# Optimization experiments

Measured on AMD Instinct MI355X. Metric: run time of the kernel, lower is better.

Reference implementation:

```python
import jax, jax.numpy as jnp
import numpy as np

B, T, C = 4, 2048, 1024
N_HEAD = 16
HEAD_DIM = C // N_HEAD
SCALE = 1.0 / np.sqrt(HEAD_DIM).astype(np.float32)


def setup_inputs() -> dict:
    key = jax.random.key(0)
    ks = jax.random.split(key, 5)
    std = 1.0 / np.sqrt(C).astype(np.float32)
    return {
        "x": jax.random.normal(ks[0], (B, T, C), dtype=jnp.float32),
        "Wq": jax.random.normal(ks[1], (C, C), dtype=jnp.float32) * std,
        "Wk": jax.random.normal(ks[2], (C, C), dtype=jnp.float32) * std,
        "Wv": jax.random.normal(ks[3], (C, C), dtype=jnp.float32) * std,
        "Wo": jax.random.normal(ks[4], (C, C), dtype=jnp.float32) * std,
    }


def reference(x, Wq, Wk, Wv, Wo):
    # nn.Linear(x) == x @ W.T; projections then split heads: (B, H, T, D)
    def split_heads(t):
        return t.reshape(B, T, N_HEAD, HEAD_DIM).transpose(0, 2, 1, 3)

    q = split_heads(x @ Wq.T)
    k = split_heads(x @ Wk.T)
    v = split_heads(x @ Wv.T)

    att = jnp.einsum("bhqd,bhkd->bhqk", q, k) * SCALE  # (B, H, T, T)
    causal = jnp.tril(jnp.ones((T, T), dtype=bool))
    att = jnp.where(causal[None, None], att, -jnp.inf)
    att = jax.nn.softmax(att, axis=-1)
    # dropout = 0.0 (eval): identity
    y = jnp.einsum("bhqk,bhkd->bhqd", att, v)  # (B, H, T, D)
    y = y.transpose(0, 2, 1, 3).reshape(B, T, C)
    return y @ Wo.T
```

## Files before the change

kernel.cpp:

```cpp
#include <hip/hip_runtime.h>
#include <stdint.h>

#define B_SZ   4
#define T_SEQ  2048
#define C_DIM  1024
#define N_HEAD 16
#define HEAD_D 64
#define QSCALE 0.18033688011112042f

typedef unsigned short u16;
typedef unsigned int   u32;
typedef __bf16  bfv8  __attribute__((ext_vector_type(8)));
typedef float   f32x4 __attribute__((ext_vector_type(4)));

__device__ __forceinline__ u16 f2bf_hu(float f) {
  union { float f; u32 i; } u; u.f = f;
  return (u16)((u.i + 0x8000u) >> 16);
}
__device__ __forceinline__ u32 pkbf16(float a, float b) {
  union { float f; u32 i; } ua, ub; ua.f = a; ub.f = b;
  return __builtin_amdgcn_perm(ub.i + 0x8000u, ua.i + 0x8000u, 0x07060302u);
}
__device__ __forceinline__ float fexp2(float x) {
#if __has_builtin(__builtin_amdgcn_exp2f)
  return __builtin_amdgcn_exp2f(x);
#else
  return __expf(x * 0.69314718f);
#endif
}

__device__ __forceinline__ void async_cp16(const u16* __restrict__ g, u16* l) {
  __builtin_amdgcn_global_load_lds(
      (const __attribute__((address_space(1))) void*)g,
      (__attribute__((address_space(3))) void*)l, 16, 0, 0);
}

__global__ __launch_bounds__(256) void cvt_all_kernel(
    const float* __restrict__ x,  const float* __restrict__ W0,
    const float* __restrict__ W1, const float* __restrict__ W2,
    const float* __restrict__ W3, u16* __restrict__ dst) {
  int bid = blockIdx.x;
  const float* s; u16* d; int local;
  if (bid < 8192) {
    s = x; d = dst; local = bid;
  } else {
    int w = (bid - 8192) >> 10;
    local  = (bid - 8192) & 1023;
    s = (w == 0) ? W0 : (w == 1) ? W1 : (w == 2) ? W2 : W3;
    d = dst + (size_t)(B_SZ * T_SEQ * C_DIM) + (size_t)w * (C_DIM * C_DIM);
  }
  int i = local * 256 + threadIdx.x;
  float4 v = ((const float4*)s)[i];
  int2 o; o.x = (int)pkbf16(v.x, v.y); o.y = (int)pkbf16(v.z, v.w);
  ((int2*)d)[i] = o;
}

__device__ __forceinline__ void mfma_step(const u16* Sbuf, int wm, int wn,
                                          int frow, int fk, f32x4 acc[4][4]) {
  const u16* As = Sbuf;
  const u16* Bs = Sbuf + 4096;
  bfv8 af[4], bfr[4];
#pragma unroll
  for (int mt = 0; mt < 4; mt++)
    af[mt] = *(const bfv8*)(As + (wm * 64 + mt * 16 + frow) * 32 + fk);
#pragma unroll
  for (int nt = 0; nt < 4; nt++)
    bfr[nt] = *(const bfv8*)(Bs + (wn * 64 + nt * 16 + frow) * 32 + fk);
  __builtin_amdgcn_s_setprio(1);
#pragma unroll
  for (int mt = 0; mt < 4; mt++)
#pragma unroll
    for (int nt = 0; nt < 4; nt++)
      acc[mt][nt] = __builtin_amdgcn_mfma_f32_16x16x32_bf16(
          af[mt], bfr[nt], acc[mt][nt], 0, 0, 0);
  __builtin_amdgcn_s_setprio(0);
}

__device__ __forceinline__ void gemm_core(const u16* __restrict__ A,
                                          const u16* __restrict__ Bw,
                                          int m0, int n0,
                                          f32x4 acc[4][4],
                                          u16* smem) {
  const int tid  = threadIdx.x;
  const int wave = tid >> 6;
  const int lane = tid & 63;
  const int frow = lane & 15;
  const int fk   = (lane >> 4) * 8;
  const int wm   = wave >> 1, wn = wave & 1;

  const int lrow = tid >> 2;
  const int lcol = (tid & 3) * 8;
  const u16* ga0 = A  + (size_t)(m0 + lrow)      * C_DIM + lcol;
  const u16* ga1 = A  + (size_t)(m0 + 64 + lrow) * C_DIM + lcol;
  const u16* gb0 = Bw + (size_t)(n0 + lrow)      * C_DIM + lcol;
  const u16* gb1 = Bw + (size_t)(n0 + 64 + lrow) * C_DIM + lcol;
  u16* b0 = smem;
  u16* b1 = smem + 8192;
  u16* b2 = smem + 16384;
  const int so = tid * 8;

#define STAGE_TO(dst) do {                        \
    async_cp16(ga0, (dst) + so);                  \
    async_cp16(ga1, (dst) + 2048 + so);           \
    async_cp16(gb0, (dst) + 4096 + so);           \
    async_cp16(gb1, (dst) + 6144 + so);           \
    ga0 += 32; ga1 += 32; gb0 += 32; gb1 += 32;   \
  } while (0)
#define WAIT4_BAR do {                                      \
    asm volatile("s_waitcnt vmcnt(4)" ::: "memory");        \
    __builtin_amdgcn_s_barrier();                           \
  } while (0)

  STAGE_TO(b0);
  STAGE_TO(b1);
  WAIT4_BAR;

#pragma unroll 1
  for (int ii = 0; ii < 30; ii += 3) {
    STAGE_TO(b2);
    mfma_step(b0, wm, wn, frow, fk, acc);
    WAIT4_BAR;

    STAGE_TO(b0);
    mfma_step(b1, wm, wn, frow, fk, acc);
    WAIT4_BAR;

    STAGE_TO(b1);
    mfma_step(b2, wm, wn, frow, fk, acc);
    WAIT4_BAR;
  }
  mfma_step(b0, wm, wn, frow, fk, acc);
  asm volatile("s_waitcnt vmcnt(0)" ::: "memory");
  __builtin_amdgcn_s_barrier();
  mfma_step(b1, wm, wn, frow, fk, acc);
#undef STAGE_TO
#undef WAIT4_BAR
}

__global__ __launch_bounds__(256) void gemm_qkv_kernel(
    const u16* __restrict__ X, const u16* __restrict__ Wq,
    const u16* __restrict__ Wk, const u16* __restrict__ Wv,
    u16* __restrict__ Qo, u16* __restrict__ Ko, u16* __restrict__ Vo) {
  __shared__ __align__(16) u16 smem[24576];
  const u16* W = (blockIdx.z == 0) ? Wq : (blockIdx.z == 1) ? Wk : Wv;
  u16* dst     = (blockIdx.z == 0) ? Qo : (blockIdx.z == 1) ? Ko : Vo;
  const int m0 = blockIdx.x * 128, n0 = blockIdx.y * 128;

  f32x4 acc[4][4];
#pragma unroll
  for (int i = 0; i < 4; i++)
#pragma unroll
    for (int j = 0; j < 4; j++) acc[i][j] = {0.f, 0.f, 0.f, 0.f};

  gemm_core(X, W, m0, n0, acc, smem);
  __syncthreads();

  const int lane = threadIdx.x & 63, wave = threadIdx.x >> 6;
  const int wm = wave >> 1, wn = wave & 1;
  const int quad = lane >> 4, col = lane & 15;
  u16* buf = smem + wave * 4096;
  const int bb = (m0 + wm * 64) >> 11;
  const int t0 = (m0 + wm * 64) & (T_SEQ - 1);
  const int h  = (n0 >> 6) + wn;

  if (blockIdx.z == 2) {
#pragma unroll
    for (int mt = 0; mt < 4; mt++)
#pragma unroll
      for (int nt = 0; nt < 4; nt++) {
        int d_l = nt * 16 + col;
        int g   = mt * 4 + quad;
        int gp  = g ^ (d_l & 15);
        int2 o;
        o.x = (int)pkbf16(acc[mt][nt][0], acc[mt][nt][1]);
        o.y = (int)pkbf16(acc[mt][nt][2], acc[mt][nt][3]);
        *(int2*)(buf + d_l * 64 + gp * 4) = o;
      }
#pragma unroll
    for (int tt = 0; tt < 8; tt++) {
      int d_l = tt * 8 + (lane >> 3);
      int seg = lane & 7;
      int g0 = (2 * seg) ^ (d_l & 15), g1 = (2 * seg + 1) ^ (d_l & 15);
      int2 a  = *(const int2*)(buf + d_l * 64 + g0 * 4);
      int2 bv = *(const int2*)(buf + d_l * 64 + g1 * 4);
      int4 o; o.x = a.x; o.y = a.y; o.z = bv.x; o.w = bv.y;
      *(int4*)(Vo + (((size_t)(bb * N_HEAD + h) * HEAD_D + d_l) * T_SEQ
                     + t0 + seg * 8)) = o;
    }
  } else {
    const float sc = (blockIdx.z == 0) ? QSCALE : 1.0f;
#pragma unroll
    for (int mt = 0; mt < 4; mt++)
#pragma unroll
      for (int nt = 0; nt < 4; nt++)
#pragma unroll
        for (int r = 0; r < 4; r++) {
          int m_l = mt * 16 + quad * 4 + r;
          int n_l = nt * 16 + col;
          int gp = (n_l >> 3) ^ (m_l & 7);
          buf[m_l * 64 + gp * 8 + (n_l & 7)] = f2bf_hu(acc[mt][nt][r] * sc);
        }
#pragma unroll
    for (int tt = 0; tt < 8; tt++) {
      int m_l = tt * 8 + (lane >> 3);
      int seg = lane & 7;
      int gp = seg ^ (m_l & 7);
      int4 o = *(const int4*)(buf + m_l * 64 + gp * 8);
      *(int4*)(dst + (((size_t)(bb * N_HEAD + h) * T_SEQ + t0 + m_l) * HEAD_D
                      + seg * 8)) = o;
    }
  }
}

__global__ __launch_bounds__(256) void gemm_out_kernel(
    const u16* __restrict__ Y, const u16* __restrict__ Wo,
    float* __restrict__ Out) {
  __shared__ __align__(16) u16 smem[24576];
  const int m0 = blockIdx.x * 128, n0 = blockIdx.y * 128;

  f32x4 acc[4][4];
#pragma unroll
  for (int i = 0; i < 4; i++)
#pragma unroll
    for (int j = 0; j < 4; j++) acc[i][j] = {0.f, 0.f, 0.f, 0.f};

  gemm_core(Y, Wo, m0, n0, acc, smem);
  __syncthreads();

  const int lane = threadIdx.x & 63, wave = threadIdx.x >> 6;
  const int wm = wave >> 1, wn = wave & 1;
  const int quad = lane >> 4, col = lane & 15;
  float* bufF = (float*)(smem + wave * 4096);

#pragma unroll
  for (int c = 0; c < 2; c++) {
#pragma unroll
    for (int mt = 0; mt < 4; mt++)
#pragma unroll
      for (int nn = 0; nn < 2; nn++)
#pragma unroll
        for (int r = 0; r < 4; r++) {
          int nt = 2 * c + nn;
          int m_l = mt * 16 + quad * 4 + r;
          int n_l = nn * 16 + col;
          int gp = (n_l >> 2) ^ (m_l & 7);
          bufF[m_l * 32 + gp * 4 + (n_l & 3)] = acc[mt][nt][r];
        }
#pragma unroll
    for (int tt = 0; tt < 8; tt++) {
      int m_l = tt * 8 + (lane >> 3);
      int seg = lane & 7;
      int gp = seg ^ (m_l & 7);
      float4 o = *(const float4*)(bufF + m_l * 32 + gp * 4);
      *(float4*)(Out + (size_t)(m0 + wm * 64 + m_l) * C_DIM
                 + n0 + wn * 64 + c * 32 + seg * 4) = o;
    }
  }
}

#define ATT_Q 128

__global__ __launch_bounds__(256, 4) void attn_kernel(
    const u16* __restrict__ Qg, const u16* __restrict__ Kg,
    const u16* __restrict__ Vtg, u16* __restrict__ Yg) {
  __shared__ __align__(16) u16 QPs[128 * 64];
  __shared__ __align__(16) u16 Ks[64 * 64];
  __shared__ __align__(16) u16 Vt[64 * 64];

  const int tid = threadIdx.x;
  const int wave = tid >> 6, lane = tid & 63;
  const int quad = lane >> 4, l15 = lane & 15;
  const int bh = blockIdx.x;
  const int b = bh >> 4, h = bh & 15;
  const int yy = blockIdx.y, gq = yy >> 2, rq = yy & 3;
  const int qt = (gq == 0) ? 15 - rq : (gq == 1) ? rq
               : (gq == 2) ? 11 - rq : 4 + rq;
  const int q0 = qt * ATT_Q;

  {
    const int row = tid >> 1;
    const int c0 = (tid & 1) * 32;
    const u16* gp = Qg + ((size_t)bh * T_SEQ + q0 + row) * HEAD_D + c0;
#pragma unroll
    for (int g = 0; g < 4; g++) {
      int4 v = *(const int4*)(gp + g * 8);
      int pg = ((c0 >> 3) + g) ^ (row & 7);
      *(int4*)(QPs + row * 64 + pg * 8) = v;
    }
  }
  __syncthreads();

  bfv8 qb[2][2];
#pragma unroll
  for (int nt = 0; nt < 2; nt++)
#pragma unroll
    for (int ks = 0; ks < 2; ks++) {
      int q = wave * 32 + nt * 16 + l15;
      int pg = (ks * 4 + quad) ^ (q & 7);
      qb[nt][ks] = *(const bfv8*)(QPs + q * 64 + pg * 8);
    }

  float l_i[2] = {0.f, 0.f};
  f32x4 ao[4][2];
#pragma unroll
  for (int mt = 0; mt < 4; mt++)
#pragma unroll
    for (int nt = 0; nt < 2; nt++) ao[mt][nt] = {0.f, 0.f, 0.f, 0.f};

  const int srow = tid >> 2;
  const int sc0 = (tid & 3) * 16;
  const u16* gkb = Kg  + (size_t)bh * T_SEQ * HEAD_D + (size_t)srow * HEAD_D + sc0;
  const u16* gvb = Vtg + (size_t)bh * HEAD_D * T_SEQ + (size_t)srow * T_SEQ + sc0;
  const int pg0 = (sc0 >> 3) ^ (srow & 7), pg1 = ((sc0 >> 3) + 1) ^ (srow & 7);

  int4 kr0, kr1, vr0, vr1;
  kr0 = *(const int4*)(gkb);      kr1 = *(const int4*)(gkb + 8);
  vr0 = *(const int4*)(gvb);      vr1 = *(const int4*)(gvb + 8);

  const int ktmax = 2 * qt + 1;
  for (int kt = 0; kt <= ktmax; kt++) {
    __syncthreads();
    *(int4*)(Ks + srow * 64 + pg0 * 8) = kr0;
    *(int4*)(Ks + srow * 64 + pg1 * 8) = kr1;
    *(int4*)(Vt + srow * 64 + pg0 * 8) = vr0;
    *(int4*)(Vt + srow * 64 + pg1 * 8) = vr1;
    __syncthreads();
    if (kt < ktmax) {
      const u16* gk = gkb + (size_t)(kt + 1) * 64 * HEAD_D;
      const u16* gv = gvb + (kt + 1) * 64;
      kr0 = *(const int4*)(gk);  kr1 = *(const int4*)(gk + 8);
      vr0 = *(const int4*)(gv);  vr1 = *(const int4*)(gv + 8);
    }

    f32x4 as[4][2];
#pragma unroll
    for (int mt = 0; mt < 4; mt++)
#pragma unroll
      for (int nt = 0; nt < 2; nt++) as[mt][nt] = {0.f, 0.f, 0.f, 0.f};
#pragma unroll
    for (int mt = 0; mt < 4; mt++) {
      bfv8 ka[2];
#pragma unroll
      for (int ks = 0; ks < 2; ks++) {
        int key = mt * 16 + l15;
        int pg = (ks * 4 + quad) ^ (key & 7);
        ka[ks] = *(const bfv8*)(Ks + key * 64 + pg * 8);
      }
#pragma unroll
      for (int nt = 0; nt < 2; nt++)
#pragma unroll
        for (int ks = 0; ks < 2; ks++)
          as[mt][nt] = __builtin_amdgcn_mfma_f32_16x16x32_bf16(
              ka[ks], qb[nt][ks], as[mt][nt], 0, 0, 0);
    }

    const bool diag = (kt >= 2 * qt);
#pragma unroll
    for (int nt = 0; nt < 2; nt++) {
      const int q_l = wave * 32 + nt * 16 + l15;
      const int q_g = q0 + q_l;
      float lacc = 0.f;
#pragma unroll
      for (int mt = 0; mt < 4; mt++) {
        float p[4];
#pragma unroll
        for (int r = 0; r < 4; r++) {
          float s = as[mt][nt][r];
          if (diag) {
            int key_g = kt * 64 + mt * 16 + quad * 4 + r;
            if (key_g > q_g) s = -1e30f;
          }
          p[r] = fexp2(s);
        }
        lacc += (p[0] + p[1]) + (p[2] + p[3]);
        int pg = (2 * mt + (quad >> 1)) ^ (q_l & 7);
        int2 o;
        o.x = (int)pkbf16(p[0], p[1]);
        o.y = (int)pkbf16(p[2], p[3]);
        *(int2*)(QPs + q_l * 64 + pg * 8 + (quad & 1) * 4) = o;
      }
      l_i[nt] += lacc;
    }

    bfv8 pf[2][2];
#pragma unroll
    for (int nt = 0; nt < 2; nt++)
#pragma unroll
      for (int ks = 0; ks < 2; ks++) {
        int q_l = wave * 32 + nt * 16 + l15;
        int pg = (ks * 4 + quad) ^ (q_l & 7);
        pf[nt][ks] = *(const bfv8*)(QPs + q_l * 64 + pg * 8);
      }
#pragma unroll
    for (int mt = 0; mt < 4; mt++) {
      bfv8 va[2];
#pragma unroll
      for (int ks = 0; ks < 2; ks++) {
        int d = mt * 16 + l15;
        int pg = (ks * 4 + quad) ^ (d & 7);
        va[ks] = *(const bfv8*)(Vt + d * 64 + pg * 8);
      }
#pragma unroll
      for (int nt = 0; nt < 2; nt++)
#pragma unroll
        for (int ks = 0; ks < 2; ks++)
          ao[mt][nt] = __builtin_amdgcn_mfma_f32_16x16x32_bf16(
              va[ks], pf[nt][ks], ao[mt][nt], 0, 0, 0);
    }
  }

#pragma unroll
  for (int nt = 0; nt < 2; nt++) {
    l_i[nt] += __shfl_xor(l_i[nt], 16);
    l_i[nt] += __shfl_xor(l_i[nt], 32);
  }

  __syncthreads();
#pragma unroll
  for (int nt = 0; nt < 2; nt++) {
    float inv = 1.0f / l_i[nt];
    int q_l = wave * 32 + nt * 16 + l15;
#pragma unroll
    for (int mt = 0; mt < 4; mt++) {
      int g = mt * 4 + quad;
      int gp = g ^ (q_l & 15);
      int2 o;
      o.x = (int)pkbf16(ao[mt][nt][0] * inv, ao[mt][nt][1] * inv);
      o.y = (int)pkbf16(ao[mt][nt][2] * inv, ao[mt][nt][3] * inv);
      *(int2*)(QPs + q_l * 64 + gp * 4) = o;
    }
  }
  __syncthreads();
#pragma unroll
  for (int rr = 0; rr < 4; rr++) {
    int q   = rr * 32 + (tid >> 3);
    int seg = tid & 7;
    int g0 = (2 * seg) ^ (q & 15), g1 = (2 * seg + 1) ^ (q & 15);
    int2 a  = *(const int2*)(QPs + q * 64 + g0 * 4);
    int2 bv = *(const int2*)(QPs + q * 64 + g1 * 4);
    int4 o; o.x = a.x; o.y = a.y; o.z = bv.x; o.w = bv.y;
    *(int4*)(Yg + ((size_t)b * T_SEQ + q0 + q) * C_DIM + h * HEAD_D + seg * 8) = o;
  }
}

extern "C" void kernel_launch(void* const* d_in, const int* in_sizes, int n_in,
                              void* d_out, int out_size, void* d_ws, size_t ws_size,
                              hipStream_t stream) {
  const float* x  = (const float*)d_in[0];
  const float* Wq = (const float*)d_in[1];
  const float* Wk = (const float*)d_in[2];
  const float* Wv = (const float*)d_in[3];
  const float* Wo = (const float*)d_in[4];
  float* out = (float*)d_out;

  const size_t NE = (size_t)B_SZ * T_SEQ * C_DIM;
  const size_t NW = (size_t)C_DIM * C_DIM;
  u16* xbf = (u16*)d_ws;
  u16* wqb = xbf + NE;
  u16* wkb = wqb + NW;
  u16* wvb = wkb + NW;
  u16* wob = wvb + NW;
  u16* qws = wob + NW;
  u16* kws = qws + NE;
  u16* vws = kws + NE;
  u16* yws = vws + NE;

  cvt_all_kernel<<<8192 + 4096, 256, 0, stream>>>(x, Wq, Wk, Wv, Wo, xbf);

  dim3 g1(T_SEQ * B_SZ / 128, C_DIM / 128, 3);
  gemm_qkv_kernel<<<g1, 256, 0, stream>>>(xbf, wqb, wkb, wvb, qws, kws, vws);

  dim3 g2(B_SZ * N_HEAD, T_SEQ / ATT_Q);
  attn_kernel<<<g2, 256, 0, stream>>>(qws, kws, vws, yws);

  dim3 g3(T_SEQ * B_SZ / 128, C_DIM / 128);
  gemm_out_kernel<<<g3, 256, 0, stream>>>(yws, wob, out);
}
```

Baseline: 238.6 us.

## Double-buffer K/V tiles in LDS with async global-to-LDS copies

The attention kernel now stages each 64-key K and V^T tile straight from global memory into LDS with async 16-byte copies, and keeps two LDS slots so the next tile loads while the current one is being computed. This replaces the register-staged loads and the two barriers per iteration with one vmcnt wait and one barrier per iteration. The aim is to hide global load latency and cut synchronisation. The extra LDS buffers lower the launch-bounds occupancy hint from 4 to 3 blocks per CU, which may reduce latency hiding across blocks.

```diff
diff --git a/kernel.cpp b/kernel.cpp
--- a/kernel.cpp
+++ b/kernel.cpp
@@ -260,12 +260,12 @@
 
 #define ATT_Q 128
 
-__global__ __launch_bounds__(256, 4) void attn_kernel(
+__global__ __launch_bounds__(256, 3) void attn_kernel(
     const u16* __restrict__ Qg, const u16* __restrict__ Kg,
     const u16* __restrict__ Vtg, u16* __restrict__ Yg) {
   __shared__ __align__(16) u16 QPs[128 * 64];
-  __shared__ __align__(16) u16 Ks[64 * 64];
-  __shared__ __align__(16) u16 Vt[64 * 64];
+  __shared__ __align__(16) u16 Ks[2 * 64 * 64];
+  __shared__ __align__(16) u16 Vt[2 * 64 * 64];
 
   const int tid = threadIdx.x;
   const int wave = tid >> 6, lane = tid & 63;
@@ -277,6 +277,24 @@
                : (gq == 2) ? 11 - rq : 4 + rq;
   const int q0 = qt * ATT_Q;
 
+  const u16* Kbase = Kg  + (size_t)bh * T_SEQ * HEAD_D;
+  const u16* Vbase = Vtg + (size_t)bh * HEAD_D * T_SEQ;
+  const int trow = tid >> 3;
+  const int gx   = (tid & 7) ^ (trow & 7);
+
+#define STAGE_KV(slot, kt_) do {                                          \
+    const u16* ks0 = Kbase + (size_t)(((kt_) << 6) + trow) * HEAD_D + gx * 8; \
+    const u16* vs0 = Vbase + (size_t)trow * T_SEQ + ((kt_) << 6) + gx * 8;    \
+    u16* kd = Ks + (slot) * 4096 + tid * 8;                               \
+    u16* vd = Vt + (slot) * 4096 + tid * 8;                               \
+    async_cp16(ks0, kd);                                                  \
+    async_cp16(ks0 + 32 * HEAD_D, kd + 2048);                             \
+    async_cp16(vs0, vd);                                                  \
+    async_cp16(vs0 + (size_t)32 * T_SEQ, vd + 2048);                      \
+  } while (0)
+
+  STAGE_KV(0, 0);
+
   {
     const int row = tid >> 1;
     const int c0 = (tid & 1) * 32;
@@ -307,30 +325,11 @@
 #pragma unroll
     for (int nt = 0; nt < 2; nt++) ao[mt][nt] = {0.f, 0.f, 0.f, 0.f};
 
-  const int srow = tid >> 2;
-  const int sc0 = (tid & 3) * 16;
-  const u16* gkb = Kg  + (size_t)bh * T_SEQ * HEAD_D + (size_t)srow * HEAD_D + sc0;
-  const u16* gvb = Vtg + (size_t)bh * HEAD_D * T_SEQ + (size_t)srow * T_SEQ + sc0;
-  const int pg0 = (sc0 >> 3) ^ (srow & 7), pg1 = ((sc0 >> 3) + 1) ^ (srow & 7);
-
-  int4 kr0, kr1, vr0, vr1;
-  kr0 = *(const int4*)(gkb);      kr1 = *(const int4*)(gkb + 8);
-  vr0 = *(const int4*)(gvb);      vr1 = *(const int4*)(gvb + 8);
-
   const int ktmax = 2 * qt + 1;
   for (int kt = 0; kt <= ktmax; kt++) {
-    __syncthreads();
-    *(int4*)(Ks + srow * 64 + pg0 * 8) = kr0;
-    *(int4*)(Ks + srow * 64 + pg1 * 8) = kr1;
-    *(int4*)(Vt + srow * 64 + pg0 * 8) = vr0;
-    *(int4*)(Vt + srow * 64 + pg1 * 8) = vr1;
-    __syncthreads();
-    if (kt < ktmax) {
-      const u16* gk = gkb + (size_t)(kt + 1) * 64 * HEAD_D;
-      const u16* gv = gvb + (kt + 1) * 64;
-      kr0 = *(const int4*)(gk);  kr1 = *(const int4*)(gk + 8);
-      vr0 = *(const int4*)(gv);  vr1 = *(const int4*)(gv + 8);
-    }
+    if (kt < ktmax) STAGE_KV((kt + 1) & 1, kt + 1);
+    const u16* Ksb = Ks + (kt & 1) * 4096;
+    const u16* Vtb = Vt + (kt & 1) * 4096;
 
     f32x4 as[4][2];
 #pragma unroll
@@ -344,7 +343,7 @@
       for (int ks = 0; ks < 2; ks++) {
         int key = mt * 16 + l15;
         int pg = (ks * 4 + quad) ^ (key & 7);
-        ka[ks] = *(const bfv8*)(Ks + key * 64 + pg * 8);
+        ka[ks] = *(const bfv8*)(Ksb + key * 64 + pg * 8);
       }
 #pragma unroll
       for (int nt = 0; nt < 2; nt++)
@@ -398,7 +397,7 @@
       for (int ks = 0; ks < 2; ks++) {
         int d = mt * 16 + l15;
         int pg = (ks * 4 + quad) ^ (d & 7);
-        va[ks] = *(const bfv8*)(Vt + d * 64 + pg * 8);
+        va[ks] = *(const bfv8*)(Vtb + d * 64 + pg * 8);
       }
 #pragma unroll
       for (int nt = 0; nt < 2; nt++)
@@ -407,7 +406,11 @@
           ao[mt][nt] = __builtin_amdgcn_mfma_f32_16x16x32_bf16(
               va[ks], pf[nt][ks], ao[mt][nt], 0, 0, 0);
     }
-  }
+
+    asm volatile("s_waitcnt vmcnt(0)" ::: "memory");
+    __builtin_amdgcn_s_barrier();
+  }
+#undef STAGE_KV
 
 #pragma unroll
   for (int nt = 0; nt < 2; nt++) {
```

New measurement: 236.3 us, median of 3. Within noise of the previous version (-1.0%).
